# Performance work log

Hardware: AMD Instinct MI355X
Metric: run time of the kernel (lower is better)

Reference implementation:

```python
import jax, jax.numpy as jnp
import numpy as np

HEADS = 8
DIM_HEAD = 64
SCALE = DIM_HEAD ** (-0.5)


def setup_inputs() -> dict:
    key = jax.random.key(0)
    k1, k2, k3 = jax.random.split(key, 3)
    b, dim, w = 8, 256, 2048
    hidden = HEADS * DIM_HEAD  # 512
    x = jax.random.normal(k1, (b, dim, w), dtype=jnp.float32)
    # Conv1d kernel-size-1 weights collapse to matrices; scale like torch init
    w_qkv = jax.random.normal(k2, (3 * hidden, dim), dtype=jnp.float32) * (1.0 / np.sqrt(dim))
    w_out = jax.random.normal(k3, (dim, hidden), dtype=jnp.float32) * (1.0 / np.sqrt(hidden))
    b_out = jnp.zeros((dim,), dtype=jnp.float32)
    return {"x": x, "w_qkv": w_qkv, "w_out": w_out, "b_out": b_out}


def reference(x, w_qkv, w_out, b_out):
    b, c, w = x.shape
    h, dh = HEADS, DIM_HEAD
    # 1x1 conv == matmul over channel dim: [3*hidden, dim] x [b, dim, w] -> [b, 3*hidden, w]
    qkv = jnp.einsum('od,bdw->bow', w_qkv, x)
    q, k, v = jnp.split(qkv, 3, axis=1)
    # 'b (h c) x -> b h c x'
    q = q.reshape(b, h, dh, w) * SCALE
    k = k.reshape(b, h, dh, w)
    v = v.reshape(b, h, dh, w)
    sim = jnp.einsum('bhdi,bhdj->bhij', q, k)          # [b, h, w, w]
    sim = sim - jax.lax.stop_gradient(sim.max(axis=-1, keepdims=True))
    attn = jax.nn.softmax(sim, axis=-1)
    out = jnp.einsum('bhij,bhdj->bhid', attn, v)        # [b, h, w, dh]
    # 'b h x c -> b (h c) x'
    out = out.transpose(0, 1, 3, 2).reshape(b, h * dh, w)
    # output 1x1 conv with bias
    return jnp.einsum('oc,bcw->bow', w_out, out) + b_out[None, :, None]
```

## Files before the change

kernel.cpp:

```cpp
#include <hip/hip_runtime.h>
#include <hip/hip_bf16.h>

typedef __bf16 bf16x8 __attribute__((ext_vector_type(8)));
typedef float f32x4 __attribute__((ext_vector_type(4)));
typedef float f32x16 __attribute__((ext_vector_type(16)));

#define MFMA16x16(a, b, c) __builtin_amdgcn_mfma_f32_16x16x32_bf16((a), (b), (c), 0, 0, 0)
#define MFMA32x32(a, b, c) __builtin_amdgcn_mfma_f32_32x32x16_bf16((a), (b), (c), 0, 0, 0)

namespace {
constexpr int BATCH = 8;
constexpr int DIMC  = 256;
constexpr int WLEN  = 2048;
constexpr int DH    = 64;
constexpr int HID   = 512;
constexpr float QSCALE = 0.125f * 1.44269504088896340736f;

constexpr size_t OFF_WQKV = 0;
constexpr size_t OFF_WOUT = 786432;
constexpr size_t OFF_XT   = 1048576;
constexpr size_t OFF_QKT  = 9437184;
constexpr size_t OFF_V    = 42991616;
constexpr size_t OFF_AT   = 59768832;
}

__device__ inline unsigned cvt_pk_bf16(float a, float b) {
  unsigned r;
  asm("v_cvt_pk_bf16_f32 %0, %1, %2" : "=v"(r) : "v"(a), "v"(b));
  return r;
}

__device__ inline void permswap(unsigned &a, unsigned &b) {
  asm("v_permlane32_swap_b32 %0, %1" : "+v"(a), "+v"(b));
}

union U4 { unsigned u[4]; bf16x8 v; };

__device__ inline void softmax_half(const f32x16 st, bf16x8 &pfa, bf16x8 &pfb) {
  float e[16];
#pragma unroll
  for (int r = 0; r < 16; ++r) e[r] = __builtin_amdgcn_exp2f(st[r]);
  unsigned w[8];
#pragma unroll
  for (int q = 0; q < 8; ++q) w[q] = cvt_pk_bf16(e[2 * q], e[2 * q + 1]);
  unsigned a0 = w[0], a1 = w[1], a2 = w[2], a3 = w[3];
  permswap(a0, a2);
  permswap(a1, a3);
  U4 ua; ua.u[0] = a0; ua.u[1] = a1; ua.u[2] = a2; ua.u[3] = a3;
  pfa = ua.v;
  unsigned b0 = w[4], b1 = w[5], b2 = w[6], b3 = w[7];
  permswap(b0, b2);
  permswap(b1, b3);
  U4 ub; ub.u[0] = b0; ub.u[1] = b1; ub.u[2] = b2; ub.u[3] = b3;
  pfb = ub.v;
}

__global__ __launch_bounds__(256) void prep_transpose(
    const float* __restrict__ x, const float* __restrict__ wqkv,
    const float* __restrict__ wout, __hip_bfloat16* __restrict__ xT,
    __hip_bfloat16* __restrict__ wqkv_bf, __hip_bfloat16* __restrict__ wout_bf) {
  int tid = threadIdx.x;
  if (blockIdx.z == 8) {
    int flat = (blockIdx.y * 32 + blockIdx.x) * 256 + tid;
#pragma unroll
    for (int it = 0; it < 12; ++it) {
      int i = it * 32768 + flat;
      wqkv_bf[i] = __float2bfloat16(wqkv[i]);
    }
#pragma unroll
    for (int it = 0; it < 4; ++it) {
      int i = it * 32768 + flat;
      wout_bf[i] = __float2bfloat16(wout[i]);
    }
    return;
  }
  __shared__ float t[64][65];
  int b = blockIdx.z;
  int d0 = blockIdx.y * 64, w0 = blockIdx.x * 64;
  const float* xb = x + (size_t)b * DIMC * WLEN;
#pragma unroll
  for (int r = 0; r < 16; ++r) {
    int dd = r * 4 + (tid >> 6);
    int ww = tid & 63;
    t[dd][ww] = xb[(size_t)(d0 + dd) * WLEN + w0 + ww];
  }
  __syncthreads();
  __hip_bfloat16* xTb = xT + (size_t)b * WLEN * DIMC;
#pragma unroll
  for (int r = 0; r < 16; ++r) {
    int ww = r * 4 + (tid >> 6);
    int dd = tid & 63;
    xTb[(size_t)(w0 + ww) * DIMC + d0 + dd] = __float2bfloat16(t[dd][ww]);
  }
}

__global__ __launch_bounds__(256) void qkv_gemm(
    const __hip_bfloat16* __restrict__ wqkv_bf,
    const __hip_bfloat16* __restrict__ xT,
    __hip_bfloat16* __restrict__ qkT, __hip_bfloat16* __restrict__ vbuf) {
  int b = blockIdx.z;
  int o0 = blockIdx.y * 128, w0 = blockIdx.x * 128;
  int tid = threadIdx.x;
  int wid = tid >> 6, lane = tid & 63;
  int il = lane & 31, hi = lane >> 5;
  int wo = (wid >> 1) * 64;
  int ww = (wid & 1) * 64;

  __shared__ __align__(16) char lds_raw[36864];
  __hip_bfloat16* Al = reinterpret_cast<__hip_bfloat16*>(lds_raw);
  __hip_bfloat16* Bl = Al + 2 * 128 * 36;

  const __hip_bfloat16* xb = xT + (size_t)b * WLEN * DIMC;

  const int srow = tid >> 2;
  const int scol = (tid & 3) * 8;
  const __hip_bfloat16* asrc = wqkv_bf + (size_t)(o0 + srow) * DIMC + scol;
  const __hip_bfloat16* bsrc = xb + (size_t)(w0 + srow) * DIMC + scol;

  bf16x8 ga0, ga1, gb0, gb1;
  auto stage_load = [&](int k0) {
    ga0 = *reinterpret_cast<const bf16x8*>(asrc + k0);
    ga1 = *reinterpret_cast<const bf16x8*>(asrc + 64 * DIMC + k0);
    gb0 = *reinterpret_cast<const bf16x8*>(bsrc + k0);
    gb1 = *reinterpret_cast<const bf16x8*>(bsrc + 64 * DIMC + k0);
  };
  auto stage_write = [&](int bf) {
    *reinterpret_cast<bf16x8*>(Al + (bf * 128 + srow) * 36 + scol)      = ga0;
    *reinterpret_cast<bf16x8*>(Al + (bf * 128 + srow + 64) * 36 + scol) = ga1;
    *reinterpret_cast<bf16x8*>(Bl + (bf * 128 + srow) * 36 + scol)      = gb0;
    *reinterpret_cast<bf16x8*>(Bl + (bf * 128 + srow + 64) * 36 + scol) = gb1;
  };

  f32x16 acc[2][2];
#pragma unroll
  for (int ta = 0; ta < 2; ++ta)
#pragma unroll
    for (int tb = 0; tb < 2; ++tb)
#pragma unroll
      for (int r = 0; r < 16; ++r) acc[ta][tb][r] = 0.f;

  auto compute = [&](int cur) {
    bf16x8 af[2][2], bfr[2][2];
#pragma unroll
    for (int ta = 0; ta < 2; ++ta)
#pragma unroll
      for (int kk = 0; kk < 2; ++kk) {
        af[ta][kk] = *reinterpret_cast<const bf16x8*>(
            Al + (cur * 128 + wo + ta * 32 + il) * 36 + kk * 16 + hi * 8);
        bfr[ta][kk] = *reinterpret_cast<const bf16x8*>(
            Bl + (cur * 128 + ww + ta * 32 + il) * 36 + kk * 16 + hi * 8);
      }
    __builtin_amdgcn_s_setprio(1);
#pragma unroll
    for (int kk = 0; kk < 2; ++kk)
#pragma unroll
      for (int ta = 0; ta < 2; ++ta)
#pragma unroll
        for (int tb = 0; tb < 2; ++tb)
          acc[ta][tb] = MFMA32x32(af[ta][kk], bfr[tb][kk], acc[ta][tb]);
    __builtin_amdgcn_s_setprio(0);
  };

  stage_load(0);
  stage_write(0);
  __syncthreads();
#pragma unroll 2
  for (int t = 0; t < 7; ++t) {
    stage_load((t + 1) * 32);
    compute(t & 1);
    stage_write((t + 1) & 1);
    __syncthreads();
  }
  compute(1);
  __syncthreads();

  if (o0 < 1024) {
    float scale = (o0 < 512) ? QSCALE : 1.0f;
    __hip_bfloat16* bw = reinterpret_cast<__hip_bfloat16*>(lds_raw);
#pragma unroll
    for (int ta = 0; ta < 2; ++ta)
#pragma unroll
      for (int tb = 0; tb < 2; ++tb)
#pragma unroll
        for (int q = 0; q < 8; ++q) {
          int dl = ((2 * q) & 3) + 8 * (q >> 1) + 4 * hi;
          int row = ww + tb * 32 + il;
          int col = wo + ta * 32 + dl;
          unsigned pk = cvt_pk_bf16(acc[ta][tb][2 * q] * scale,
                                    acc[ta][tb][2 * q + 1] * scale);
          *reinterpret_cast<unsigned*>(bw + row * 136 + col) = pk;
        }
    __syncthreads();
    __hip_bfloat16* outq = qkT + (size_t)b * WLEN * 1024;
#pragma unroll
    for (int it = 0; it < 8; ++it) {
      int row = it * 16 + (tid >> 4);
      int c = (tid & 15) * 8;
      bf16x8 v = *reinterpret_cast<const bf16x8*>(bw + row * 136 + c);
      *reinterpret_cast<bf16x8*>(outq + (size_t)(w0 + row) * 1024 + o0 + c) = v;
    }
  } else {
    __hip_bfloat16* bo = reinterpret_cast<__hip_bfloat16*>(lds_raw);
#pragma unroll
    for (int ta = 0; ta < 2; ++ta)
#pragma unroll
      for (int tb = 0; tb < 2; ++tb)
#pragma unroll
        for (int r = 0; r < 16; ++r) {
          int orow = wo + ta * 32 + (r & 3) + 8 * (r >> 2) + 4 * hi;
          int wcol = ww + tb * 32 + il;
          bo[orow * 136 + wcol] = __float2bfloat16(acc[ta][tb][r]);
        }
    __syncthreads();
    __hip_bfloat16* outv = vbuf + (size_t)b * HID * WLEN;
#pragma unroll
    for (int it = 0; it < 8; ++it) {
      int orow = it * 16 + (tid >> 4);
      int c = (tid & 15) * 8;
      bf16x8 v = *reinterpret_cast<const bf16x8*>(bo + orow * 136 + c);
      *reinterpret_cast<bf16x8*>(outv + (size_t)(o0 - 1024 + orow) * WLEN + w0 + c) = v;
    }
  }
}

__global__ __launch_bounds__(256) void attn_kernel(
    const __hip_bfloat16* __restrict__ qkT,
    const __hip_bfloat16* __restrict__ vbuf,
    __hip_bfloat16* __restrict__ attnT) {
  int f = blockIdx.x;
  int xcd = f & 7, slot = f >> 3;
  int b = slot >> 4;
  int h = xcd;
  int xb = slot & 15;
  int tid = threadIdx.x, wid = tid >> 6, lane = tid & 63;
  int il = lane & 31, hi = lane >> 5;
  int i0w = xb * 128 + wid * 32;

  const __hip_bfloat16* qk_b = qkT + (size_t)b * WLEN * 1024;
  const __hip_bfloat16* vb = vbuf + (size_t)b * HID * WLEN + (size_t)h * DH * WLEN;

  __shared__ __align__(16) __hip_bfloat16 Kl[2][64][72];
  __shared__ __align__(16) __hip_bfloat16 Vl[2][64][72];

  bf16x8 qf[4];
  {
    const __hip_bfloat16* qrow = qk_b + (size_t)(i0w + il) * 1024 + h * 64 + hi * 8;
#pragma unroll
    for (int s = 0; s < 4; ++s)
      qf[s] = *reinterpret_cast<const bf16x8*>(qrow + s * 16);
  }

  bf16x8 ones;
  {
    U4 uo;
    uo.u[0] = 0x3F803F80u; uo.u[1] = 0x3F803F80u;
    uo.u[2] = 0x3F803F80u; uo.u[3] = 0x3F803F80u;
    ones = uo.v;
  }

  f32x16 oacc0, oacc1, lacc;
#pragma unroll
  for (int r = 0; r < 16; ++r) { oacc0[r] = 0.f; oacc1[r] = 0.f; lacc[r] = 0.f; }

  const int srow = tid >> 3;
  const int scol = (tid & 7) * 8;
  const __hip_bfloat16* ksrc = qk_b + 512 + h * 64 + scol;
  const __hip_bfloat16* vsrc = vb + scol;

  bf16x8 gk0, gk1, gv0, gv1;
  auto stage_load = [&](int j0) {
    gk0 = *reinterpret_cast<const bf16x8*>(ksrc + (size_t)(j0 + srow) * 1024);
    gk1 = *reinterpret_cast<const bf16x8*>(ksrc + (size_t)(j0 + srow + 32) * 1024);
    gv0 = *reinterpret_cast<const bf16x8*>(vsrc + (size_t)srow * WLEN + j0);
    gv1 = *reinterpret_cast<const bf16x8*>(vsrc + (size_t)(srow + 32) * WLEN + j0);
  };
  auto stage_write = [&](int bf) {
    *reinterpret_cast<bf16x8*>(&Kl[bf][srow][scol])      = gk0;
    *reinterpret_cast<bf16x8*>(&Kl[bf][srow + 32][scol]) = gk1;
    *reinterpret_cast<bf16x8*>(&Vl[bf][srow][scol])      = gv0;
    *reinterpret_cast<bf16x8*>(&Vl[bf][srow + 32][scol]) = gv1;
  };

  auto compute = [&](int cur) {
    f32x16 st0, st1;
#pragma unroll
    for (int r = 0; r < 16; ++r) { st0[r] = 0.f; st1[r] = 0.f; }
    __builtin_amdgcn_s_setprio(1);
#pragma unroll
    for (int s = 0; s < 4; ++s)
      st0 = MFMA32x32(*reinterpret_cast<const bf16x8*>(&Kl[cur][il][s * 16 + hi * 8]),
                      qf[s], st0);
#pragma unroll
    for (int s = 0; s < 4; ++s)
      st1 = MFMA32x32(*reinterpret_cast<const bf16x8*>(&Kl[cur][il + 32][s * 16 + hi * 8]),
                      qf[s], st1);
    __builtin_amdgcn_s_setprio(0);

    bf16x8 p0, p1, p2, p3;
    softmax_half(st0, p0, p1);
    __builtin_amdgcn_s_setprio(1);
    oacc0 = MFMA32x32(*reinterpret_cast<const bf16x8*>(&Vl[cur][il][hi * 8]),      p0, oacc0);
    oacc1 = MFMA32x32(*reinterpret_cast<const bf16x8*>(&Vl[cur][il + 32][hi * 8]), p0, oacc1);
    lacc  = MFMA32x32(ones, p0, lacc);
    oacc0 = MFMA32x32(*reinterpret_cast<const bf16x8*>(&Vl[cur][il][16 + hi * 8]),      p1, oacc0);
    oacc1 = MFMA32x32(*reinterpret_cast<const bf16x8*>(&Vl[cur][il + 32][16 + hi * 8]), p1, oacc1);
    lacc  = MFMA32x32(ones, p1, lacc);
    __builtin_amdgcn_s_setprio(0);

    softmax_half(st1, p2, p3);
    __builtin_amdgcn_s_setprio(1);
    oacc0 = MFMA32x32(*reinterpret_cast<const bf16x8*>(&Vl[cur][il][32 + hi * 8]),      p2, oacc0);
    oacc1 = MFMA32x32(*reinterpret_cast<const bf16x8*>(&Vl[cur][il + 32][32 + hi * 8]), p2, oacc1);
    lacc  = MFMA32x32(ones, p2, lacc);
    oacc0 = MFMA32x32(*reinterpret_cast<const bf16x8*>(&Vl[cur][il][48 + hi * 8]),      p3, oacc0);
    oacc1 = MFMA32x32(*reinterpret_cast<const bf16x8*>(&Vl[cur][il + 32][48 + hi * 8]), p3, oacc1);
    lacc  = MFMA32x32(ones, p3, lacc);
    __builtin_amdgcn_s_setprio(0);
  };

  stage_load(0);
  stage_write(0);
  __syncthreads();

  constexpr int NT = WLEN / 64;
#pragma unroll 1
  for (int t = 0; t < NT - 1; ++t) {
    stage_load((t + 1) * 64);
    compute(t & 1);
    stage_write((t + 1) & 1);
    __syncthreads();
  }
  compute((NT - 1) & 1);
  __syncthreads();

  float l = lacc[0];
  __hip_bfloat16* olds = &Kl[0][0][0];
  float rl = 1.0f / l;
#pragma unroll
  for (int q = 0; q < 8; ++q) {
    int dl = ((2 * q) & 3) + 8 * (q >> 1) + 4 * hi;
    unsigned pk0 = cvt_pk_bf16(oacc0[2 * q] * rl, oacc0[2 * q + 1] * rl);
    unsigned pk1 = cvt_pk_bf16(oacc1[2 * q] * rl, oacc1[2 * q + 1] * rl);
    *reinterpret_cast<unsigned*>(olds + (wid * 32 + il) * 72 + dl)      = pk0;
    *reinterpret_cast<unsigned*>(olds + (wid * 32 + il) * 72 + 32 + dl) = pk1;
  }
  __hip_bfloat16* ob = attnT + (size_t)b * WLEN * HID + h * 64;
  int dcol = (lane & 7) * 8;
#pragma unroll
  for (int it = 0; it < 4; ++it) {
    int ir = it * 8 + (lane >> 3);
    bf16x8 vrow = *reinterpret_cast<const bf16x8*>(olds + (wid * 32 + ir) * 72 + dcol);
    *reinterpret_cast<bf16x8*>(ob + (size_t)(i0w + ir) * HID + dcol) = vrow;
  }
}

__global__ __launch_bounds__(256) void out_proj(
    const __hip_bfloat16* __restrict__ attnT,
    const __hip_bfloat16* __restrict__ wout_bf,
    const float* __restrict__ b_out, float* __restrict__ out) {
  int b = blockIdx.z;
  int o0 = blockIdx.y * 128, w0 = blockIdx.x * 64;
  int tid = threadIdx.x;
  int wid = tid >> 6, lane = tid & 63;
  int il = lane & 31, hi = lane >> 5;
  int wo = (wid >> 1) * 64;
  int ww = (wid & 1) * 32;

  __shared__ __align__(16) __hip_bfloat16 Al[2][128][36];
  __shared__ __align__(16) __hip_bfloat16 Bl[2][64][36];

  const __hip_bfloat16* at_b = attnT + (size_t)b * WLEN * HID;

  const int srow = tid >> 2;
  const int scol = (tid & 3) * 8;
  const __hip_bfloat16* asrc = wout_bf + (size_t)(o0 + srow) * HID + scol;
  const __hip_bfloat16* bsrc = at_b + (size_t)(w0 + srow) * HID + scol;

  bf16x8 ga0, ga1, gb0;
  auto stage_load = [&](int k0) {
    ga0 = *reinterpret_cast<const bf16x8*>(asrc + k0);
    ga1 = *reinterpret_cast<const bf16x8*>(asrc + 64 * HID + k0);
    gb0 = *reinterpret_cast<const bf16x8*>(bsrc + k0);
  };
  auto stage_write = [&](int bf) {
    *reinterpret_cast<bf16x8*>(&Al[bf][srow][scol])      = ga0;
    *reinterpret_cast<bf16x8*>(&Al[bf][srow + 64][scol]) = ga1;
    *reinterpret_cast<bf16x8*>(&Bl[bf][srow][scol])      = gb0;
  };

  f32x16 acc[2];
#pragma unroll
  for (int ta = 0; ta < 2; ++ta)
#pragma unroll
    for (int r = 0; r < 16; ++r) acc[ta][r] = 0.f;

  auto compute = [&](int cur) {
    bf16x8 af[2][2], bfr[2];
#pragma unroll
    for (int kk = 0; kk < 2; ++kk) {
      bfr[kk] = *reinterpret_cast<const bf16x8*>(&Bl[cur][ww + il][kk * 16 + hi * 8]);
#pragma unroll
      for (int ta = 0; ta < 2; ++ta)
        af[ta][kk] = *reinterpret_cast<const bf16x8*>(
            &Al[cur][wo + ta * 32 + il][kk * 16 + hi * 8]);
    }
    __builtin_amdgcn_s_setprio(1);
#pragma unroll
    for (int kk = 0; kk < 2; ++kk)
#pragma unroll
      for (int ta = 0; ta < 2; ++ta)
        acc[ta] = MFMA32x32(af[ta][kk], bfr[kk], acc[ta]);
    __builtin_amdgcn_s_setprio(0);
  };

  stage_load(0);
  stage_write(0);
  __syncthreads();
#pragma unroll 2
  for (int t = 0; t < 15; ++t) {
    stage_load((t + 1) * 32);
    compute(t & 1);
    stage_write((t + 1) & 1);
    __syncthreads();
  }
  compute(1);

  float* outb = out + (size_t)b * DIMC * WLEN;
#pragma unroll
  for (int ta = 0; ta < 2; ++ta)
#pragma unroll
    for (int r = 0; r < 16; ++r) {
      int og = o0 + wo + ta * 32 + (r & 3) + 8 * (r >> 2) + 4 * hi;
      int wg = w0 + ww + il;
      outb[(size_t)og * WLEN + wg] = acc[ta][r] + b_out[og];
    }
}

extern "C" void kernel_launch(void* const* d_in, const int* in_sizes, int n_in,
                              void* d_out, int out_size, void* d_ws, size_t ws_size,
                              hipStream_t stream) {
  const float* x    = (const float*)d_in[0];
  const float* wqkv = (const float*)d_in[1];
  const float* wout = (const float*)d_in[2];
  const float* bout = (const float*)d_in[3];
  float* out = (float*)d_out;
  char* ws = (char*)d_ws;

  __hip_bfloat16* wqkv_bf = (__hip_bfloat16*)(ws + OFF_WQKV);
  __hip_bfloat16* wout_bf = (__hip_bfloat16*)(ws + OFF_WOUT);
  __hip_bfloat16* xT      = (__hip_bfloat16*)(ws + OFF_XT);
  __hip_bfloat16* qkT     = (__hip_bfloat16*)(ws + OFF_QKT);
  __hip_bfloat16* vbuf    = (__hip_bfloat16*)(ws + OFF_V);
  __hip_bfloat16* attnT   = (__hip_bfloat16*)(ws + OFF_AT);

  prep_transpose<<<dim3(WLEN / 64, DIMC / 64, 9), dim3(256), 0, stream>>>(
      x, wqkv, wout, xT, wqkv_bf, wout_bf);
  qkv_gemm<<<dim3(WLEN / 128, 1536 / 128, BATCH), dim3(256), 0, stream>>>(wqkv_bf, xT, qkT, vbuf);
  attn_kernel<<<dim3(1024), dim3(256), 0, stream>>>(qkT, vbuf, attnT);
  out_proj<<<dim3(WLEN / 64, DIMC / 128, BATCH), dim3(256), 0, stream>>>(attnT, wout_bf, bout, out);
}
```

Baseline: 178.5 us.

## Stage K/V tiles via async global_load_lds with XOR-swizzled LDS layout

Replaces the register-staged global-to-LDS copy of K and V tiles with direct global_load_lds async copies into a double-buffered LDS area. The padded [64][72] layout becomes an unpadded 64-wide layout with an XOR column swizzle to avoid bank conflicts. This removes the VGPRs that held prefetched data and the ds_write instructions. It relies on the barrier to order the async writes, so it risks a race if the compiler does not insert the needed vmcnt waits.

```diff
diff --git a/kernel.cpp b/kernel.cpp
--- a/kernel.cpp
+++ b/kernel.cpp
@@ -32,6 +32,13 @@
 
 __device__ inline void permswap(unsigned &a, unsigned &b) {
   asm("v_permlane32_swap_b32 %0, %1" : "+v"(a), "+v"(b));
+}
+
+__device__ inline void async_copy16(void* lds, const void* g) {
+  __builtin_amdgcn_global_load_lds(
+      (const __attribute__((address_space(1))) void*)g,
+      (__attribute__((address_space(3))) void*)lds,
+      16, 0, 0);
 }
 
 union U4 { unsigned u[4]; bf16x8 v; };
@@ -239,8 +246,9 @@
   const __hip_bfloat16* qk_b = qkT + (size_t)b * WLEN * 1024;
   const __hip_bfloat16* vb = vbuf + (size_t)b * HID * WLEN + (size_t)h * DH * WLEN;
 
-  __shared__ __align__(16) __hip_bfloat16 Kl[2][64][72];
-  __shared__ __align__(16) __hip_bfloat16 Vl[2][64][72];
+  __shared__ __align__(16) char araw[32768];
+  __hip_bfloat16* Ke = reinterpret_cast<__hip_bfloat16*>(araw);
+  __hip_bfloat16* Ve = reinterpret_cast<__hip_bfloat16*>(araw + 16384);
 
   bf16x8 qf[4];
   {
@@ -262,85 +270,87 @@
 #pragma unroll
   for (int r = 0; r < 16; ++r) { oacc0[r] = 0.f; oacc1[r] = 0.f; lacc[r] = 0.f; }
 
-  const int srow = tid >> 3;
-  const int scol = (tid & 7) * 8;
-  const __hip_bfloat16* ksrc = qk_b + 512 + h * 64 + scol;
-  const __hip_bfloat16* vsrc = vb + scol;
-
-  bf16x8 gk0, gk1, gv0, gv1;
-  auto stage_load = [&](int j0) {
-    gk0 = *reinterpret_cast<const bf16x8*>(ksrc + (size_t)(j0 + srow) * 1024);
-    gk1 = *reinterpret_cast<const bf16x8*>(ksrc + (size_t)(j0 + srow + 32) * 1024);
-    gv0 = *reinterpret_cast<const bf16x8*>(vsrc + (size_t)srow * WLEN + j0);
-    gv1 = *reinterpret_cast<const bf16x8*>(vsrc + (size_t)(srow + 32) * WLEN + j0);
-  };
-  auto stage_write = [&](int bf) {
-    *reinterpret_cast<bf16x8*>(&Kl[bf][srow][scol])      = gk0;
-    *reinterpret_cast<bf16x8*>(&Kl[bf][srow + 32][scol]) = gk1;
-    *reinterpret_cast<bf16x8*>(&Vl[bf][srow][scol])      = gv0;
-    *reinterpret_cast<bf16x8*>(&Vl[bf][srow + 32][scol]) = gv1;
-  };
+  const int rl = lane >> 3;
+  const int srow8 = wid * 8 + rl;
+  const int csw = ((lane & 7) ^ rl) * 8;
+  const __hip_bfloat16* kS = qk_b + 512 + h * 64 + csw;
+  const __hip_bfloat16* vS = vb + (size_t)srow8 * WLEN + csw;
+
+  auto stage = [&](int buf, int j0) {
+    char* kd = araw + buf * 8192 + wid * 1024;
+    char* vd = araw + 16384 + buf * 8192 + wid * 1024;
+    async_copy16(kd,        kS + (size_t)(j0 + srow8) * 1024);
+    async_copy16(kd + 4096, kS + (size_t)(j0 + 32 + srow8) * 1024);
+    async_copy16(vd,        vS + j0);
+    async_copy16(vd + 4096, vS + 32 * WLEN + j0);
+  };
+
+  const int kx = il & 7;
 
   auto compute = [&](int cur) {
+    const __hip_bfloat16* kb = Ke + cur * 4096;
+    const __hip_bfloat16* vl = Ve + cur * 4096;
     f32x16 st0, st1;
 #pragma unroll
     for (int r = 0; r < 16; ++r) { st0[r] = 0.f; st1[r] = 0.f; }
     __builtin_amdgcn_s_setprio(1);
 #pragma unroll
-    for (int s = 0; s < 4; ++s)
-      st0 = MFMA32x32(*reinterpret_cast<const bf16x8*>(&Kl[cur][il][s * 16 + hi * 8]),
-                      qf[s], st0);
-#pragma unroll
-    for (int s = 0; s < 4; ++s)
-      st1 = MFMA32x32(*reinterpret_cast<const bf16x8*>(&Kl[cur][il + 32][s * 16 + hi * 8]),
-                      qf[s], st1);
+    for (int s = 0; s < 4; ++s) {
+      int c = ((s * 2 + hi) ^ kx) * 8;
+      st0 = MFMA32x32(*reinterpret_cast<const bf16x8*>(kb + il * 64 + c), qf[s], st0);
+      st1 = MFMA32x32(*reinterpret_cast<const bf16x8*>(kb + (il + 32) * 64 + c), qf[s], st1);
+    }
     __builtin_amdgcn_s_setprio(0);
 
     bf16x8 p0, p1, p2, p3;
     softmax_half(st0, p0, p1);
-    __builtin_amdgcn_s_setprio(1);
-    oacc0 = MFMA32x32(*reinterpret_cast<const bf16x8*>(&Vl[cur][il][hi * 8]),      p0, oacc0);
-    oacc1 = MFMA32x32(*reinterpret_cast<const bf16x8*>(&Vl[cur][il + 32][hi * 8]), p0, oacc1);
-    lacc  = MFMA32x32(ones, p0, lacc);
-    oacc0 = MFMA32x32(*reinterpret_cast<const bf16x8*>(&Vl[cur][il][16 + hi * 8]),      p1, oacc0);
-    oacc1 = MFMA32x32(*reinterpret_cast<const bf16x8*>(&Vl[cur][il + 32][16 + hi * 8]), p1, oacc1);
-    lacc  = MFMA32x32(ones, p1, lacc);
-    __builtin_amdgcn_s_setprio(0);
+    {
+      int c0 = ((0 + hi) ^ kx) * 8, c1 = ((2 + hi) ^ kx) * 8;
+      __builtin_amdgcn_s_setprio(1);
+      oacc0 = MFMA32x32(*reinterpret_cast<const bf16x8*>(vl + il * 64 + c0),        p0, oacc0);
+      oacc1 = MFMA32x32(*reinterpret_cast<const bf16x8*>(vl + (il + 32) * 64 + c0), p0, oacc1);
+      lacc  = MFMA32x32(ones, p0, lacc);
+      oacc0 = MFMA32x32(*reinterpret_cast<const bf16x8*>(vl + il * 64 + c1),        p1, oacc0);
+      oacc1 = MFMA32x32(*reinterpret_cast<const bf16x8*>(vl + (il + 32) * 64 + c1), p1, oacc1);
+      lacc  = MFMA32x32(ones, p1, lacc);
+      __builtin_amdgcn_s_setprio(0);
+    }
 
     softmax_half(st1, p2, p3);
-    __builtin_amdgcn_s_setprio(1);
-    oacc0 = MFMA32x32(*reinterpret_cast<const bf16x8*>(&Vl[cur][il][32 + hi * 8]),      p2, oacc0);
-    oacc1 = MFMA32x32(*reinterpret_cast<const bf16x8*>(&Vl[cur][il + 32][32 + hi * 8]), p2, oacc1);
-    lacc  = MFMA32x32(ones, p2, lacc);
-    oacc0 = MFMA32x32(*reinterpret_cast<const bf16x8*>(&Vl[cur][il][48 + hi * 8]),      p3, oacc0);
-    oacc1 = MFMA32x32(*reinterpret_cast<const bf16x8*>(&Vl[cur][il + 32][48 + hi * 8]), p3, oacc1);
-    lacc  = MFMA32x32(ones, p3, lacc);
-    __builtin_amdgcn_s_setprio(0);
-  };
-
-  stage_load(0);
-  stage_write(0);
+    {
+      int c2 = ((4 + hi) ^ kx) * 8, c3 = ((6 + hi) ^ kx) * 8;
+      __builtin_amdgcn_s_setprio(1);
+      oacc0 = MFMA32x32(*reinterpret_cast<const bf16x8*>(vl + il * 64 + c2),        p2, oacc0);
+      oacc1 = MFMA32x32(*reinterpret_cast<const bf16x8*>(vl + (il + 32) * 64 + c2), p2, oacc1);
+      lacc  = MFMA32x32(ones, p2, lacc);
+      oacc0 = MFMA32x32(*reinterpret_cast<const bf16x8*>(vl + il * 64 + c3),        p3, oacc0);
+      oacc1 = MFMA32x32(*reinterpret_cast<const bf16x8*>(vl + (il + 32) * 64 + c3), p3, oacc1);
+      lacc  = MFMA32x32(ones, p3, lacc);
+      __builtin_amdgcn_s_setprio(0);
+    }
+  };
+
+  stage(0, 0);
   __syncthreads();
 
   constexpr int NT = WLEN / 64;
 #pragma unroll 1
   for (int t = 0; t < NT - 1; ++t) {
-    stage_load((t + 1) * 64);
+    stage((t + 1) & 1, (t + 1) * 64);
     compute(t & 1);
-    stage_write((t + 1) & 1);
     __syncthreads();
   }
   compute((NT - 1) & 1);
   __syncthreads();
 
   float l = lacc[0];
-  __hip_bfloat16* olds = &Kl[0][0][0];
-  float rl = 1.0f / l;
+  __hip_bfloat16* olds = reinterpret_cast<__hip_bfloat16*>(araw);
+  float rl2 = 1.0f / l;
 #pragma unroll
   for (int q = 0; q < 8; ++q) {
     int dl = ((2 * q) & 3) + 8 * (q >> 1) + 4 * hi;
-    unsigned pk0 = cvt_pk_bf16(oacc0[2 * q] * rl, oacc0[2 * q + 1] * rl);
-    unsigned pk1 = cvt_pk_bf16(oacc1[2 * q] * rl, oacc1[2 * q + 1] * rl);
+    unsigned pk0 = cvt_pk_bf16(oacc0[2 * q] * rl2, oacc0[2 * q + 1] * rl2);
+    unsigned pk1 = cvt_pk_bf16(oacc1[2 * q] * rl2, oacc1[2 * q + 1] * rl2);
     *reinterpret_cast<unsigned*>(olds + (wid * 32 + il) * 72 + dl)      = pk0;
     *reinterpret_cast<unsigned*>(olds + (wid * 32 + il) * 72 + 32 + dl) = pk1;
   }
```

New measurement: 178.1 us, median of 2. Within noise of the previous version (-0.2%).
